# Performance work log

Hardware: AMD Instinct MI355X
Metric: run time of the kernel (lower is better)

## Reference

```python
import jax, jax.numpy as jnp
import numpy as np

B, S, D, H, P, KN = 32, 197, 768, 12, 196, 32
HD = D // H
DFF = 4 * D


def layer_norm(x, g, b, eps=1e-5):
    mu = jnp.mean(x, axis=-1, keepdims=True)
    var = jnp.var(x, axis=-1, keepdims=True)
    return (x - mu) * jax.lax.rsqrt(var + eps) * g + b


def setup_inputs() -> dict:
    key = jax.random.key(0)
    ks = jax.random.split(key, 16)
    s = 0.02
    return {
        "x": jax.random.normal(ks[0], (B, S, D), dtype=jnp.float32),
        "routes": jax.random.randint(ks[1], (P, KN), 0, P, dtype=jnp.int32),
        "qkv_w": jax.random.normal(ks[2], (D, 3 * D), dtype=jnp.float32) * s,
        "qkv_b": jnp.zeros((3 * D,), jnp.float32),
        "proj_w": jax.random.normal(ks[3], (D, D), dtype=jnp.float32) * s,
        "proj_b": jnp.zeros((D,), jnp.float32),
        "n1_g": jnp.ones((D,), jnp.float32),
        "n1_b": jnp.zeros((D,), jnp.float32),
        "n2_g": jnp.ones((D,), jnp.float32),
        "n2_b": jnp.zeros((D,), jnp.float32),
        "mlp_w1": jax.random.normal(ks[4], (D, DFF), dtype=jnp.float32) * s,
        "mlp_b1": jnp.zeros((DFF,), jnp.float32),
        "mlp_w2": jax.random.normal(ks[5], (DFF, D), dtype=jnp.float32) * s,
        "mlp_b2": jnp.zeros((D,), jnp.float32),
    }


def reference(x, routes, qkv_w, qkv_b, proj_w, proj_b, n1_g, n1_b, n2_g, n2_b,
              mlp_w1, mlp_b1, mlp_w2, mlp_b2):
    scale = HD ** -0.5
    x_norm = layer_norm(x, n1_g, n1_b)
    qkv = (x_norm @ qkv_w + qkv_b).reshape(B, S, 3, H, HD)
    qkv = jnp.transpose(qkv, (2, 0, 3, 1, 4))  # [3,B,H,S,hd]
    Q, K, V = qkv[0], qkv[1], qkv[2]

    # CLS: dense attention over all S tokens
    scores_cls = jnp.einsum('bhqd,bhkd->bhqk', Q[:, :, :1], K) * scale
    attn_cls = jax.nn.softmax(scores_cls, axis=-1)
    out_cls = jnp.einsum('bhqk,bhkd->bhqd', attn_cls, V)  # [B,H,1,hd]

    # Patches: sparse attention over k routed neighbors (shift +1 skips CLS)
    routes_shifted = routes + 1  # [P,k], indices into S
    K_g = jnp.take(K, routes_shifted, axis=2)  # [B,H,P,k,hd]
    V_g = jnp.take(V, routes_shifted, axis=2)
    scores_p = jnp.einsum('bhpd,bhpkd->bhpk', Q[:, :, 1:], K_g) * scale
    attn_p = jax.nn.softmax(scores_p, axis=-1)
    out_p = jnp.einsum('bhpk,bhpkd->bhpd', attn_p, V_g)  # [B,H,P,hd]

    out = jnp.concatenate([out_cls, out_p], axis=2)  # [B,H,S,hd]
    out = jnp.transpose(out, (0, 2, 1, 3)).reshape(B, S, D)
    out = out @ proj_w + proj_b
    x = x + out

    h = layer_norm(x, n2_g, n2_b)
    h = jax.nn.gelu(h @ mlp_w1 + mlp_b1, approximate=False)
    x = x + (h @ mlp_w2 + mlp_b2)
    return x
```

## Files before the change

### kernel.cpp

```cpp
#include <hip/hip_runtime.h>
#include <hip/hip_bf16.h>
#include <math.h>

#define B_ 32
#define S_ 197
#define D_ 768
#define H_ 12
#define P_ 196
#define KN_ 32
#define HD_ 64
#define DFF_ 3072
#define M_ (B_ * S_)

typedef __attribute__((ext_vector_type(8))) short short8;
typedef __attribute__((ext_vector_type(8))) __bf16 bf16x8;
typedef __attribute__((ext_vector_type(4))) float f32x4;
typedef __attribute__((ext_vector_type(4))) float float4v;

static __device__ __forceinline__ unsigned short f2bf(float f) {
    unsigned u = __builtin_bit_cast(unsigned, f);
    u += 0x7FFFu + ((u >> 16) & 1u);
    return (unsigned short)(u >> 16);
}
static __device__ __forceinline__ float bf2f(unsigned short s) {
    unsigned u = ((unsigned)s) << 16;
    return __builtin_bit_cast(float, u);
}

static __device__ __forceinline__ void gload_lds16(const void* g, void* l) {
    __builtin_amdgcn_global_load_lds(
        (const __attribute__((address_space(1))) unsigned int*)g,
        (__attribute__((address_space(3))) unsigned int*)l, 16, 0, 0);
}

__global__ void __launch_bounds__(256) cvt_t_kernel(const float* __restrict__ in,
        unsigned short* __restrict__ out, int K, int N) {
    __shared__ float tile[32][33];
    int nt = N >> 5;
    int bx = blockIdx.x % nt;
    int by = blockIdx.x / nt;
    int n0 = bx << 5, k0 = by << 5;
    int tx = threadIdx.x & 31, ty = threadIdx.x >> 5;
    #pragma unroll
    for (int i = 0; i < 32; i += 8)
        tile[ty + i][tx] = in[(size_t)(k0 + ty + i) * N + n0 + tx];
    __syncthreads();
    #pragma unroll
    for (int i = 0; i < 32; i += 8)
        out[(size_t)(n0 + ty + i) * K + k0 + tx] = f2bf(tile[tx][ty + i]);
}

__global__ void __launch_bounds__(256) ln_kernel(const float* __restrict__ x,
        const float* __restrict__ g, const float* __restrict__ bt,
        unsigned short* __restrict__ out) {
    int row = blockIdx.x;
    int tid = threadIdx.x;
    const float* xr = x + (size_t)row * D_;
    float v0 = xr[tid], v1 = xr[tid + 256], v2 = xr[tid + 512];
    float s = v0 + v1 + v2;
    float q = v0 * v0 + v1 * v1 + v2 * v2;
    #pragma unroll
    for (int o = 32; o >= 1; o >>= 1) {
        s += __shfl_xor(s, o);
        q += __shfl_xor(q, o);
    }
    __shared__ float red[8];
    int wave = tid >> 6, lane = tid & 63;
    if (lane == 0) { red[wave] = s; red[4 + wave] = q; }
    __syncthreads();
    float S0 = red[0] + red[1] + red[2] + red[3];
    float Q0 = red[4] + red[5] + red[6] + red[7];
    float mean = S0 * (1.0f / D_);
    float var = Q0 * (1.0f / D_) - mean * mean;
    float rstd = rsqrtf(var + 1e-5f);
    unsigned short* orow = out + (size_t)row * D_;
    orow[tid]       = f2bf((v0 - mean) * rstd * g[tid]       + bt[tid]);
    orow[tid + 256] = f2bf((v1 - mean) * rstd * g[tid + 256] + bt[tid + 256]);
    orow[tid + 512] = f2bf((v2 - mean) * rstd * g[tid + 512] + bt[tid + 512]);
}

template<int BM, int BN, int EPI>
__global__ void __launch_bounds__(256) gemm_kernel(
        const unsigned short* __restrict__ A,
        const unsigned short* __restrict__ Bt,
        const float* __restrict__ bias,
        const float* __restrict__ resid,
        void* __restrict__ outp,
        int M, int N, int K) {
    constexpr int BK = 64;
    constexpr int WM = BM / 2, WN = BN / 2;
    constexpr int MR = WM / 16, NR = WN / 16;
    constexpr int ACH = BM / 8;
    constexpr int BCH = BN / 8;
    __shared__ short As[BM * BK];
    __shared__ short Bs[BN * BK];

    int nwg = gridDim.x;
    int orig = blockIdx.x;
    int q8 = nwg >> 3, r8 = nwg & 7;
    int xcd = orig & 7, idx = orig >> 3;
    int wg = (xcd < r8 ? xcd * (q8 + 1) : r8 * (q8 + 1) + (xcd - r8) * q8) + idx;

    int ntn = N / BN;
    int bm = (wg / ntn) * BM;
    int bn = (wg % ntn) * BN;
    int tid = threadIdx.x;
    int lane = tid & 63;
    int wave = tid >> 6;
    int wm = (wave >> 1) * WM, wn = (wave & 1) * WN;
    int lr = lane & 15;
    int lk0 = (lane >> 4) << 3;
    int crow = lane >> 3;
    int ccol = (lane & 7) << 3;

    f32x4 acc[MR][NR] = {};

    for (int kt = 0; kt < K; kt += BK) {
        #pragma unroll
        for (int c = wave; c < ACH; c += 4) {
            int grow = bm + c * 8 + crow;
            if (grow >= M) grow = M - 1;
            gload_lds16(A + (size_t)grow * K + kt + ccol, &As[c * 512]);
        }
        #pragma unroll
        for (int c = wave; c < BCH; c += 4) {
            int grow = bn + c * 8 + crow;
            gload_lds16(Bt + (size_t)grow * K + kt + ccol, &Bs[c * 512]);
        }
        __syncthreads();
        #pragma unroll
        for (int kk = 0; kk < 2; ++kk) {
            int lk = lk0 + kk * 32;
            bf16x8 af[MR], bfv[NR];
            #pragma unroll
            for (int m = 0; m < MR; ++m)
                af[m] = __builtin_bit_cast(bf16x8,
                    *(short8*)(&As[(wm + m * 16 + lr) * BK + lk]));
            #pragma unroll
            for (int n = 0; n < NR; ++n)
                bfv[n] = __builtin_bit_cast(bf16x8,
                    *(short8*)(&Bs[(wn + n * 16 + lr) * BK + lk]));
            #pragma unroll
            for (int m = 0; m < MR; ++m)
                #pragma unroll
                for (int n = 0; n < NR; ++n)
                    acc[m][n] = __builtin_amdgcn_mfma_f32_16x16x32_bf16(
                        af[m], bfv[n], acc[m][n], 0, 0, 0);
        }
        __syncthreads();
    }

    int r0 = (lane >> 4) << 2;
    #pragma unroll
    for (int m = 0; m < MR; ++m) {
        #pragma unroll
        for (int n = 0; n < NR; ++n) {
            int col = bn + wn + n * 16 + lr;
            #pragma unroll
            for (int r = 0; r < 4; ++r) {
                int row = bm + wm + m * 16 + r0 + r;
                if (row < M) {
                    float v = acc[m][n][r] + bias[col];
                    if (EPI == 1)
                        v = 0.5f * v * (1.0f + erff(v * 0.70710678118f));
                    if (EPI == 2) {
                        ((float*)outp)[(size_t)row * N + col] =
                            v + resid[(size_t)row * N + col];
                    } else {
                        ((unsigned short*)outp)[(size_t)row * N + col] = f2bf(v);
                    }
                }
            }
        }
    }
}

__global__ void __launch_bounds__(256) attn_patch_kernel(
        const unsigned short* __restrict__ qkv,
        const int* __restrict__ routes,
        unsigned short* __restrict__ out) {
    int wid = (blockIdx.x * 256 + threadIdx.x) >> 6;
    int lane = threadIdx.x & 63;
    int b = wid / (H_ * P_);
    int rem = wid - b * (H_ * P_);
    int h = rem / P_;
    int p = rem - h * P_;
    int ks = lane & 31, half = lane >> 5;
    int skey = routes[p * KN_ + ks] + 1;
    const unsigned short* Qrow = qkv + (size_t)(b * S_ + p + 1) * (3 * D_) + h * HD_;
    const unsigned short* Krow = qkv + (size_t)(b * S_ + skey) * (3 * D_) + D_ + h * HD_;
    float dot = 0.f;
    #pragma unroll
    for (int q = 0; q < 4; ++q) {
        short8 qv = *(const short8*)(Qrow + half * 32 + q * 8);
        short8 kv = *(const short8*)(Krow + half * 32 + q * 8);
        #pragma unroll
        for (int j = 0; j < 8; ++j)
            dot += bf2f((unsigned short)qv[j]) * bf2f((unsigned short)kv[j]);
    }
    dot += __shfl_xor(dot, 32);
    float sc = dot * 0.125f;
    float mx = sc;
    #pragma unroll
    for (int o = 16; o >= 1; o >>= 1) mx = fmaxf(mx, __shfl_xor(mx, o));
    float e = __expf(sc - mx);
    float ssum = e;
    #pragma unroll
    for (int o = 16; o >= 1; o >>= 1) ssum += __shfl_xor(ssum, o);
    float w = e / ssum;
    const unsigned short* Vb = qkv + (size_t)b * S_ * (3 * D_) + 2 * D_ + h * HD_;
    float o_acc = 0.f;
    #pragma unroll 4
    for (int k = 0; k < 32; ++k) {
        float wk = __shfl(w, k);
        int sk = __shfl(skey, k);
        o_acc += wk * bf2f(Vb[(size_t)sk * (3 * D_) + lane]);
    }
    out[(size_t)(b * S_ + p + 1) * D_ + h * HD_ + lane] = f2bf(o_acc);
}

__global__ void __launch_bounds__(256) attn_cls_kernel(
        const unsigned short* __restrict__ qkv,
        unsigned short* __restrict__ out) {
    int wid = (blockIdx.x * 256 + threadIdx.x) >> 6;
    int lane = threadIdx.x & 63;
    int b = wid / H_, h = wid - b * H_;
    int ks = lane & 31, half = lane >> 5;
    const unsigned short* base = qkv + (size_t)b * S_ * (3 * D_);
    const unsigned short* Qrow = base + h * HD_;
    short8 qv[4];
    #pragma unroll
    for (int q = 0; q < 4; ++q)
        qv[q] = *(const short8*)(Qrow + half * 32 + q * 8);
    float sc[7];
    #pragma unroll
    for (int c = 0; c < 7; ++c) {
        int key = c * 32 + ks;
        float dot = 0.f;
        if (key < S_) {
            const unsigned short* Krow =
                base + (size_t)key * (3 * D_) + D_ + h * HD_ + half * 32;
            #pragma unroll
            for (int q = 0; q < 4; ++q) {
                short8 kv = *(const short8*)(Krow + q * 8);
                #pragma unroll
                for (int j = 0; j < 8; ++j)
                    dot += bf2f((unsigned short)qv[q][j]) * bf2f((unsigned short)kv[j]);
            }
        }
        dot += __shfl_xor(dot, 32);
        sc[c] = (key < S_) ? dot * 0.125f : -1e30f;
    }
    float mx = -1e30f;
    #pragma unroll
    for (int c = 0; c < 7; ++c) mx = fmaxf(mx, sc[c]);
    #pragma unroll
    for (int o = 16; o >= 1; o >>= 1) mx = fmaxf(mx, __shfl_xor(mx, o));
    float e[7];
    float ssum = 0.f;
    #pragma unroll
    for (int c = 0; c < 7; ++c) { e[c] = __expf(sc[c] - mx); ssum += e[c]; }
    #pragma unroll
    for (int o = 16; o >= 1; o >>= 1) ssum += __shfl_xor(ssum, o);
    float inv = 1.f / ssum;
    const unsigned short* Vb = base + 2 * D_ + h * HD_;
    float o_acc = 0.f;
    for (int c = 0; c < 7; ++c) {
        for (int k = 0; k < 32; ++k) {
            int key = c * 32 + k;
            if (key < S_) {
                float wk = __shfl(e[c], k) * inv;
                o_acc += wk * bf2f(Vb[(size_t)key * (3 * D_) + lane]);
            }
        }
    }
    out[(size_t)(b * S_) * D_ + h * HD_ + lane] = f2bf(o_acc);
}

extern "C" void kernel_launch(void* const* d_in, const int* in_sizes, int n_in,
                              void* d_out, int out_size, void* d_ws, size_t ws_size,
                              hipStream_t stream) {
    const float* x      = (const float*)d_in[0];
    const int*   routes = (const int*)d_in[1];
    const float* qkv_w  = (const float*)d_in[2];
    const float* qkv_b  = (const float*)d_in[3];
    const float* proj_w = (const float*)d_in[4];
    const float* proj_b = (const float*)d_in[5];
    const float* n1_g   = (const float*)d_in[6];
    const float* n1_b   = (const float*)d_in[7];
    const float* n2_g   = (const float*)d_in[8];
    const float* n2_b   = (const float*)d_in[9];
    const float* w1     = (const float*)d_in[10];
    const float* b1     = (const float*)d_in[11];
    const float* w2     = (const float*)d_in[12];
    const float* b2     = (const float*)d_in[13];
    float* out = (float*)d_out;

    char* ws = (char*)d_ws;
    size_t off = 0;
    auto alloc = [&](size_t bytes) -> void* {
        void* p = ws + off;
        off += (bytes + 255) & ~(size_t)255;
        return p;
    };
    unsigned short* wq_bf  = (unsigned short*)alloc((size_t)D_ * 3 * D_ * 2);
    unsigned short* wp_bf  = (unsigned short*)alloc((size_t)D_ * D_ * 2);
    unsigned short* w1_bf  = (unsigned short*)alloc((size_t)D_ * DFF_ * 2);
    unsigned short* w2_bf  = (unsigned short*)alloc((size_t)DFF_ * D_ * 2);
    unsigned short* xn_bf  = (unsigned short*)alloc((size_t)M_ * D_ * 2);
    float*          x1     = (float*)alloc((size_t)M_ * D_ * 4);
    unsigned short* qkv_bf = (unsigned short*)alloc((size_t)M_ * 3 * D_ * 2);
    unsigned short* attn_bf= (unsigned short*)alloc((size_t)M_ * D_ * 2);
    unsigned short* h_bf   = qkv_bf;

    auto cvt_t = [&](const float* src, unsigned short* dst, int K, int N) {
        cvt_t_kernel<<<(N >> 5) * (K >> 5), 256, 0, stream>>>(src, dst, K, N);
    };
    cvt_t(qkv_w, wq_bf, D_, 3 * D_);
    cvt_t(proj_w, wp_bf, D_, D_);
    cvt_t(w1, w1_bf, D_, DFF_);
    cvt_t(w2, w2_bf, DFF_, D_);

    ln_kernel<<<M_, 256, 0, stream>>>(x, n1_g, n1_b, xn_bf);

    gemm_kernel<128, 128, 0><<<50 * (3 * D_ / 128), 256, 0, stream>>>(
        xn_bf, wq_bf, qkv_b, nullptr, qkv_bf, M_, 3 * D_, D_);

    attn_patch_kernel<<<(B_ * H_ * P_) / 4, 256, 0, stream>>>(qkv_bf, routes, attn_bf);
    attn_cls_kernel<<<(B_ * H_) / 4, 256, 0, stream>>>(qkv_bf, attn_bf);

    gemm_kernel<128, 64, 2><<<50 * (D_ / 64), 256, 0, stream>>>(
        attn_bf, wp_bf, proj_b, x, x1, M_, D_, D_);

    ln_kernel<<<M_, 256, 0, stream>>>(x1, n2_g, n2_b, xn_bf);

    gemm_kernel<128, 128, 1><<<50 * (DFF_ / 128), 256, 0, stream>>>(
        xn_bf, w1_bf, b1, nullptr, h_bf, M_, DFF_, D_);

    gemm_kernel<128, 64, 2><<<50 * (D_ / 64), 256, 0, stream>>>(
        h_bf, w2_bf, b2, x1, out, M_, D_, DFF_);
}
```

Baseline: 446.0 us.

## Double-buffer GEMM LDS tiles with XOR swizzle and MFMA priority boost

The GEMM mainloop now uses two LDS buffers, so the next K tile is fetched with direct global-to-LDS loads while MFMAs run on the current tile. Each thread's load offset is XOR-swizzled by row, and the reads apply a matching swizzle to avoid LDS bank conflicts. Wave priority is raised around the MFMA section. LDS use doubles, which may lower occupancy for the larger tile configurations.

```diff
diff --git a/kernel.cpp b/kernel.cpp
--- a/kernel.cpp
+++ b/kernel.cpp
@@ -92,8 +92,9 @@
     constexpr int MR = WM / 16, NR = WN / 16;
     constexpr int ACH = BM / 8;
     constexpr int BCH = BN / 8;
-    __shared__ short As[BM * BK];
-    __shared__ short Bs[BN * BK];
+    constexpr int ASZ = BM * BK, BSZ = BN * BK;
+    __shared__ short As[2 * ASZ];
+    __shared__ short Bs[2 * BSZ];
 
     int nwg = gridDim.x;
     int orig = blockIdx.x;
@@ -111,35 +112,49 @@
     int lr = lane & 15;
     int lk0 = (lane >> 4) << 3;
     int crow = lane >> 3;
-    int ccol = (lane & 7) << 3;
+    int scol = (((lane & 7) ^ ((lane >> 3) & 7)) << 3);
+    int rsw = (lr & 7) << 3;
 
     f32x4 acc[MR][NR] = {};
 
-    for (int kt = 0; kt < K; kt += BK) {
+    auto stage = [&](int kt, int buf) {
+        short* Ad = &As[buf * ASZ];
+        short* Bd = &Bs[buf * BSZ];
         #pragma unroll
         for (int c = wave; c < ACH; c += 4) {
             int grow = bm + c * 8 + crow;
             if (grow >= M) grow = M - 1;
-            gload_lds16(A + (size_t)grow * K + kt + ccol, &As[c * 512]);
+            gload_lds16(A + (size_t)grow * K + kt + scol, &Ad[c * 512]);
         }
         #pragma unroll
         for (int c = wave; c < BCH; c += 4) {
             int grow = bn + c * 8 + crow;
-            gload_lds16(Bt + (size_t)grow * K + kt + ccol, &Bs[c * 512]);
-        }
-        __syncthreads();
+            gload_lds16(Bt + (size_t)grow * K + kt + scol, &Bd[c * 512]);
+        }
+    };
+
+    int nt = K / BK;
+    stage(0, 0);
+    __syncthreads();
+
+    for (int t = 0; t < nt; ++t) {
+        int cur = t & 1;
+        if (t + 1 < nt) stage((t + 1) * BK, cur ^ 1);
+        const short* Ab = &As[cur * ASZ];
+        const short* Bb = &Bs[cur * BSZ];
+        __builtin_amdgcn_s_setprio(1);
         #pragma unroll
         for (int kk = 0; kk < 2; ++kk) {
-            int lk = lk0 + kk * 32;
+            int lkb = lk0 + kk * 32;
             bf16x8 af[MR], bfv[NR];
             #pragma unroll
             for (int m = 0; m < MR; ++m)
                 af[m] = __builtin_bit_cast(bf16x8,
-                    *(short8*)(&As[(wm + m * 16 + lr) * BK + lk]));
+                    *(const short8*)(&Ab[(wm + m * 16 + lr) * BK + (lkb ^ rsw)]));
             #pragma unroll
             for (int n = 0; n < NR; ++n)
                 bfv[n] = __builtin_bit_cast(bf16x8,
-                    *(short8*)(&Bs[(wn + n * 16 + lr) * BK + lk]));
+                    *(const short8*)(&Bb[(wn + n * 16 + lr) * BK + (lkb ^ rsw)]));
             #pragma unroll
             for (int m = 0; m < MR; ++m)
                 #pragma unroll
@@ -147,6 +162,7 @@
                     acc[m][n] = __builtin_amdgcn_mfma_f32_16x16x32_bf16(
                         af[m], bfv[n], acc[m][n], 0, 0, 0);
         }
+        __builtin_amdgcn_s_setprio(0);
         __syncthreads();
     }
 
```

New measurement: 430.7 us. 1.04x faster.
